# Kernel tuning notes

Measured on AMD Instinct MI355X. Metric: run time of the kernel, lower is better.

Reference implementation:

```python
import jax, jax.numpy as jnp
import numpy as np

B, T, I, H, L, C = 8192, 50, 50, 10, 3, 5


def setup_inputs() -> dict:
    key = jax.random.key(0)
    ks = jax.random.split(key, 20)
    s = 1.0 / np.sqrt(H)  # torch nn.RNN init scale
    inp = {
        "x": jax.random.normal(ks[0], (B, T, I), dtype=jnp.float32),
        "h0": jax.random.normal(ks[1], (L, B, H), dtype=jnp.float32),
    }
    # per-layer weights: layer 0 takes input_size I, layers 1,2 take H
    in_sizes = [I, H, H]
    for l in range(L):
        inp[f"W_ih{l}"] = jax.random.uniform(ks[2 + 4 * l], (H, in_sizes[l]), minval=-s, maxval=s, dtype=jnp.float32)
        inp[f"W_hh{l}"] = jax.random.uniform(ks[3 + 4 * l], (H, H), minval=-s, maxval=s, dtype=jnp.float32)
        inp[f"b_ih{l}"] = jax.random.uniform(ks[4 + 4 * l], (H,), minval=-s, maxval=s, dtype=jnp.float32)
        inp[f"b_hh{l}"] = jax.random.uniform(ks[5 + 4 * l], (H,), minval=-s, maxval=s, dtype=jnp.float32)
    sf = 1.0 / np.sqrt(H * T)
    inp["fc_w"] = jax.random.uniform(ks[14], (C, H * T), minval=-sf, maxval=sf, dtype=jnp.float32)
    inp["fc_b"] = jax.random.uniform(ks[15], (C,), minval=-sf, maxval=sf, dtype=jnp.float32)
    return inp


def _rnn_layer(x, h0, W_ih, b_ih, W_hh, b_hh):
    # x: [B, T, in], h0: [B, H]. h_t = tanh(x_t W_ih^T + b_ih + h_{t-1} W_hh^T + b_hh)
    xW = jnp.einsum("bti,hi->bth", x, W_ih) + (b_ih + b_hh)  # input proj precomputed

    def step(h, xw_t):
        h = jnp.tanh(xw_t + h @ W_hh.T)
        return h, h

    _, ys = jax.lax.scan(step, h0, jnp.swapaxes(xW, 0, 1))  # ys: [T, B, H]
    return jnp.swapaxes(ys, 0, 1)  # [B, T, H]


def reference(x, h0, W_ih0, W_hh0, b_ih0, b_hh0, W_ih1, W_hh1, b_ih1, b_hh1,
              W_ih2, W_hh2, b_ih2, b_hh2, fc_w, fc_b):
    layers = [(W_ih0, b_ih0, W_hh0, b_hh0),
              (W_ih1, b_ih1, W_hh1, b_hh1),
              (W_ih2, b_ih2, W_hh2, b_hh2)]
    out = x
    for l, (Wi, bi, Wh, bh) in enumerate(layers):
        out = _rnn_layer(out, h0[l], Wi, bi, Wh, bh)
    flat = jax.nn.relu(out.reshape(out.shape[0], -1))  # [B, T*H]
    return flat @ fc_w.T + fc_b  # [B, C]
```

## Files before the change

kernel.cpp:

```cpp
#include <hip/hip_runtime.h>

#define BB 8192
#define TT 50
#define II 50
#define HH 10
#define CC 5

__device__ __forceinline__ float fast_tanh(float x) {
    float e = __expf(2.0f * x);
    return 1.0f - 2.0f * __builtin_amdgcn_rcpf(e + 1.0f);
}

__global__ __launch_bounds__(256) void k_proj0(
    const float* __restrict__ x, const float* __restrict__ Wih0,
    const float* __restrict__ bih0, const float* __restrict__ bhh0,
    float* __restrict__ P) {
    int gid = blockIdx.x * 256 + threadIdx.x;
    int b = gid & (BB - 1);
    int t = gid >> 13;
    const float2* xr = (const float2*)(x + ((size_t)b * TT + t) * II);
    float2 xv[II / 2];
#pragma unroll
    for (int i = 0; i < II / 2; i++) xv[i] = xr[i];
#pragma unroll
    for (int j = 0; j < HH; j++) {
        float a = bih0[j] + bhh0[j];
        const float2* w = (const float2*)(Wih0 + j * II);
#pragma unroll
        for (int i = 0; i < II / 2; i++) {
            float2 wv = w[i];
            a = fmaf(wv.x, xv[i].x, a);
            a = fmaf(wv.y, xv[i].y, a);
        }
        P[((size_t)t * HH + j) * BB + b] = a;
    }
}

__global__ __launch_bounds__(256, 4) void k_fused(
    const float* __restrict__ h0all,
    const float* __restrict__ Whh0,
    const float* __restrict__ Wih1, const float* __restrict__ Whh1,
    const float* __restrict__ bih1, const float* __restrict__ bhh1,
    const float* __restrict__ Wih2, const float* __restrict__ Whh2,
    const float* __restrict__ bih2, const float* __restrict__ bhh2,
    const float* __restrict__ fcw, const float* __restrict__ fcb,
    const float* __restrict__ P, float* __restrict__ out) {
    __shared__ float sfcT[TT * HH * CC];
    __shared__ __align__(16) float sh[2][3][16][12];

    const int tid = threadIdx.x;
    const int j = tid & 15;
    const int g16 = tid >> 4;
    const int b = blockIdx.x * 16 + g16;
    const bool jv = (j < HH);

    for (int idx = tid; idx < TT * HH * CC; idx += 256) {
        int r = idx / CC, c = idx - r * CC;
        sfcT[idx] = fcw[(size_t)c * (TT * HH) + r];
    }

    float w0[HH], wi1[HH], wh1[HH], wi2[HH], wh2[HH];
    float bs1 = 0.0f, bs2 = 0.0f, h1i = 0.0f, h2i = 0.0f;
    if (jv) {
#pragma unroll
        for (int k = 0; k < HH; k++) {
            w0[k]  = Whh0[j * HH + k];
            wi1[k] = Wih1[j * HH + k];
            wh1[k] = Whh1[j * HH + k];
            wi2[k] = Wih2[j * HH + k];
            wh2[k] = Whh2[j * HH + k];
        }
        bs1 = bih1[j] + bhh1[j];
        bs2 = bih2[j] + bhh2[j];
        h1i = h0all[(size_t)BB * HH + (size_t)b * HH + j];
        h2i = h0all[(size_t)2 * BB * HH + (size_t)b * HH + j];
    } else {
#pragma unroll
        for (int k = 0; k < HH; k++) {
            w0[k] = wi1[k] = wh1[k] = wi2[k] = wh2[k] = 0.0f;
        }
    }

    if (j < 12) {
        float h0i = jv ? h0all[(size_t)b * HH + j] : 0.0f;
        sh[1][0][g16][j] = h0i;
        sh[1][1][g16][j] = (j < HH) ? h1i : 0.0f;
        sh[1][2][g16][j] = (j < HH) ? h2i : 0.0f;
    }

    __syncthreads();

    float acc[CC] = {0.0f, 0.0f, 0.0f, 0.0f, 0.0f};
    float pc = jv ? P[(size_t)j * BB + b] : 0.0f;
    float p1 = jv ? P[(size_t)(((1 < TT) ? 1 : TT - 1) * HH + j) * BB + b] : 0.0f;

#pragma unroll 1
    for (int i = 0; i < TT + 2; i++) {
        const int pr = (i + 1) & 1;
        const int pw = i & 1;

        int tp = (i + 2 < TT) ? (i + 2) : (TT - 1);
        float p2 = jv ? P[(size_t)(tp * HH + j) * BB + b] : 0.0f;

        float hv0[HH], hv1[HH], hv2[HH];
        {
            const float* b0 = &sh[pr][0][g16][0];
            const float* b1 = &sh[pr][1][g16][0];
            const float* b2 = &sh[pr][2][g16][0];
            float4 a4 = *(const float4*)(b0);
            float4 b4 = *(const float4*)(b0 + 4);
            float2 c2 = *(const float2*)(b0 + 8);
            hv0[0] = a4.x; hv0[1] = a4.y; hv0[2] = a4.z; hv0[3] = a4.w;
            hv0[4] = b4.x; hv0[5] = b4.y; hv0[6] = b4.z; hv0[7] = b4.w;
            hv0[8] = c2.x; hv0[9] = c2.y;
            a4 = *(const float4*)(b1); b4 = *(const float4*)(b1 + 4); c2 = *(const float2*)(b1 + 8);
            hv1[0] = a4.x; hv1[1] = a4.y; hv1[2] = a4.z; hv1[3] = a4.w;
            hv1[4] = b4.x; hv1[5] = b4.y; hv1[6] = b4.z; hv1[7] = b4.w;
            hv1[8] = c2.x; hv1[9] = c2.y;
            a4 = *(const float4*)(b2); b4 = *(const float4*)(b2 + 4); c2 = *(const float2*)(b2 + 8);
            hv2[0] = a4.x; hv2[1] = a4.y; hv2[2] = a4.z; hv2[3] = a4.w;
            hv2[4] = b4.x; hv2[5] = b4.y; hv2[6] = b4.z; hv2[7] = b4.w;
            hv2[8] = c2.x; hv2[9] = c2.y;
        }

        float a0 = pc, a1 = bs1, a2 = bs2;
#pragma unroll
        for (int k = 0; k < HH; k++) {
            a0 = fmaf(w0[k],  hv0[k], a0);
            a1 = fmaf(wi1[k], hv0[k], a1);
            a1 = fmaf(wh1[k], hv1[k], a1);
            a2 = fmaf(wi2[k], hv1[k], a2);
            a2 = fmaf(wh2[k], hv2[k], a2);
        }
        float h0o = fast_tanh(a0);
        float h1o = fast_tanh(a1);
        float h2o = fast_tanh(a2);

        if (i >= 2 && jv) {
            float rl = fmaxf(h2o, 0.0f);
            int base = ((i - 2) * HH + j) * CC;
#pragma unroll
            for (int c = 0; c < CC; c++) acc[c] = fmaf(sfcT[base + c], rl, acc[c]);
        }

        if (j < 12) {
            float v1 = (i == 0) ? h1i : h1o;
            float v2 = (i <= 1) ? h2i : h2o;
            sh[pw][0][g16][j] = h0o;
            sh[pw][1][g16][j] = v1;
            sh[pw][2][g16][j] = v2;
        }
        pc = p1;
        p1 = p2;
    }

#pragma unroll
    for (int c = 0; c < CC; c++) {
        float a = acc[c];
        a += __shfl_xor(a, 1);
        a += __shfl_xor(a, 2);
        a += __shfl_xor(a, 4);
        a += __shfl_xor(a, 8);
        acc[c] = a + fcb[c];
    }
    if (j == 0) {
#pragma unroll
        for (int c = 0; c < CC; c++) out[(size_t)b * CC + c] = acc[c];
    }
}

extern "C" void kernel_launch(void* const* d_in, const int* in_sizes, int n_in,
                              void* d_out, int out_size, void* d_ws, size_t ws_size,
                              hipStream_t stream) {
    const float* x    = (const float*)d_in[0];
    const float* h0   = (const float*)d_in[1];
    const float* Wih0 = (const float*)d_in[2];
    const float* Whh0 = (const float*)d_in[3];
    const float* bih0 = (const float*)d_in[4];
    const float* bhh0 = (const float*)d_in[5];
    const float* Wih1 = (const float*)d_in[6];
    const float* Whh1 = (const float*)d_in[7];
    const float* bih1 = (const float*)d_in[8];
    const float* bhh1 = (const float*)d_in[9];
    const float* Wih2 = (const float*)d_in[10];
    const float* Whh2 = (const float*)d_in[11];
    const float* bih2 = (const float*)d_in[12];
    const float* bhh2 = (const float*)d_in[13];
    const float* fcw  = (const float*)d_in[14];
    const float* fcb  = (const float*)d_in[15];
    float* out = (float*)d_out;
    float* P   = (float*)d_ws;

    k_proj0<<<(BB * TT) / 256, 256, 0, stream>>>(x, Wih0, bih0, bhh0, P);
    k_fused<<<BB / 16, 256, 0, stream>>>(h0, Whh0, Wih1, Whh1, bih1, bhh1,
                                         Wih2, Whh2, bih2, bhh2, fcw, fcb, P, out);
}
```

Before: 55.54 us.

## Broadcast hidden state via ds_swizzle instead of LDS double buffer

Replaces the shared-memory double-buffered hidden-state exchange with ds_swizzle broadcasts within each 16-lane group, so every lane reads all 10 hidden values straight from registers. This removes the LDS stores and vector loads on the recurrence's critical path. The P prefetch is deepened from 2 to 4 steps, and the fc weights are padded to stride 8 so each step can use one float4 load. Launch bounds drop the occupancy hint from 4 to 2 blocks, which allows more registers at the cost of fewer resident waves.

Result: slower. 64.15 us (+15.5%).

```diff
diff --git a/kernel.cpp b/kernel.cpp
--- a/kernel.cpp
+++ b/kernel.cpp
@@ -10,6 +10,14 @@
     float e = __expf(2.0f * x);
     return 1.0f - 2.0f * __builtin_amdgcn_rcpf(e + 1.0f);
 }
+
+#define SWZ(x, K) __uint_as_float((unsigned)__builtin_amdgcn_ds_swizzle( \
+    (int)__float_as_uint(x), (((K) << 5) | 0x10)))
+#define BC10(H, src)                                                     \
+    H[0] = SWZ(src, 0); H[1] = SWZ(src, 1); H[2] = SWZ(src, 2);          \
+    H[3] = SWZ(src, 3); H[4] = SWZ(src, 4); H[5] = SWZ(src, 5);          \
+    H[6] = SWZ(src, 6); H[7] = SWZ(src, 7); H[8] = SWZ(src, 8);          \
+    H[9] = SWZ(src, 9);
 
 __global__ __launch_bounds__(256) void k_proj0(
     const float* __restrict__ x, const float* __restrict__ Wih0,
@@ -36,7 +44,7 @@
     }
 }
 
-__global__ __launch_bounds__(256, 4) void k_fused(
+__global__ __launch_bounds__(256, 2) void k_fused(
     const float* __restrict__ h0all,
     const float* __restrict__ Whh0,
     const float* __restrict__ Wih1, const float* __restrict__ Whh1,
@@ -45,8 +53,7 @@
     const float* __restrict__ bih2, const float* __restrict__ bhh2,
     const float* __restrict__ fcw, const float* __restrict__ fcb,
     const float* __restrict__ P, float* __restrict__ out) {
-    __shared__ float sfcT[TT * HH * CC];
-    __shared__ __align__(16) float sh[2][3][16][12];
+    __shared__ __align__(16) float sfc8[TT * HH * 8];
 
     const int tid = threadIdx.x;
     const int j = tid & 15;
@@ -54,13 +61,13 @@
     const int b = blockIdx.x * 16 + g16;
     const bool jv = (j < HH);
 
-    for (int idx = tid; idx < TT * HH * CC; idx += 256) {
-        int r = idx / CC, c = idx - r * CC;
-        sfcT[idx] = fcw[(size_t)c * (TT * HH) + r];
+    for (int idx = tid; idx < TT * HH * 8; idx += 256) {
+        int r = idx >> 3, c = idx & 7;
+        sfc8[idx] = (c < CC) ? fcw[(size_t)c * (TT * HH) + r] : 0.0f;
     }
 
     float w0[HH], wi1[HH], wh1[HH], wi2[HH], wh2[HH];
-    float bs1 = 0.0f, bs2 = 0.0f, h1i = 0.0f, h2i = 0.0f;
+    float bs1 = 0.0f, bs2 = 0.0f, h1i = 0.0f, h2i = 0.0f, h0i = 0.0f;
     if (jv) {
 #pragma unroll
         for (int k = 0; k < HH; k++) {
@@ -72,6 +79,7 @@
         }
         bs1 = bih1[j] + bhh1[j];
         bs2 = bih2[j] + bhh2[j];
+        h0i = h0all[(size_t)b * HH + j];
         h1i = h0all[(size_t)BB * HH + (size_t)b * HH + j];
         h2i = h0all[(size_t)2 * BB * HH + (size_t)b * HH + j];
     } else {
@@ -81,77 +89,58 @@
         }
     }
 
-    if (j < 12) {
-        float h0i = jv ? h0all[(size_t)b * HH + j] : 0.0f;
-        sh[1][0][g16][j] = h0i;
-        sh[1][1][g16][j] = (j < HH) ? h1i : 0.0f;
-        sh[1][2][g16][j] = (j < HH) ? h2i : 0.0f;
-    }
-
     __syncthreads();
 
+    float h0o = h0i, h1o = h1i, h2o = h2i;
+
     float acc[CC] = {0.0f, 0.0f, 0.0f, 0.0f, 0.0f};
-    float pc = jv ? P[(size_t)j * BB + b] : 0.0f;
-    float p1 = jv ? P[(size_t)(((1 < TT) ? 1 : TT - 1) * HH + j) * BB + b] : 0.0f;
+
+    float p0 = jv ? P[(size_t)(0 * HH + j) * BB + b] : 0.0f;
+    float p1 = jv ? P[(size_t)(1 * HH + j) * BB + b] : 0.0f;
+    float p2 = jv ? P[(size_t)(2 * HH + j) * BB + b] : 0.0f;
+    float p3 = jv ? P[(size_t)(3 * HH + j) * BB + b] : 0.0f;
 
 #pragma unroll 1
     for (int i = 0; i < TT + 2; i++) {
-        const int pr = (i + 1) & 1;
-        const int pw = i & 1;
+        float H0[HH], H1[HH], H2[HH];
+        BC10(H0, h0o)
+        BC10(H1, h1o)
+        BC10(H2, h2o)
 
-        int tp = (i + 2 < TT) ? (i + 2) : (TT - 1);
-        float p2 = jv ? P[(size_t)(tp * HH + j) * BB + b] : 0.0f;
+        int tp = (i + 4 < TT) ? (i + 4) : (TT - 1);
+        float pnew = jv ? P[(size_t)(tp * HH + j) * BB + b] : 0.0f;
 
-        float hv0[HH], hv1[HH], hv2[HH];
-        {
-            const float* b0 = &sh[pr][0][g16][0];
-            const float* b1 = &sh[pr][1][g16][0];
-            const float* b2 = &sh[pr][2][g16][0];
-            float4 a4 = *(const float4*)(b0);
-            float4 b4 = *(const float4*)(b0 + 4);
-            float2 c2 = *(const float2*)(b0 + 8);
-            hv0[0] = a4.x; hv0[1] = a4.y; hv0[2] = a4.z; hv0[3] = a4.w;
-            hv0[4] = b4.x; hv0[5] = b4.y; hv0[6] = b4.z; hv0[7] = b4.w;
-            hv0[8] = c2.x; hv0[9] = c2.y;
-            a4 = *(const float4*)(b1); b4 = *(const float4*)(b1 + 4); c2 = *(const float2*)(b1 + 8);
-            hv1[0] = a4.x; hv1[1] = a4.y; hv1[2] = a4.z; hv1[3] = a4.w;
-            hv1[4] = b4.x; hv1[5] = b4.y; hv1[6] = b4.z; hv1[7] = b4.w;
-            hv1[8] = c2.x; hv1[9] = c2.y;
-            a4 = *(const float4*)(b2); b4 = *(const float4*)(b2 + 4); c2 = *(const float2*)(b2 + 8);
-            hv2[0] = a4.x; hv2[1] = a4.y; hv2[2] = a4.z; hv2[3] = a4.w;
-            hv2[4] = b4.x; hv2[5] = b4.y; hv2[6] = b4.z; hv2[7] = b4.w;
-            hv2[8] = c2.x; hv2[9] = c2.y;
+        int tauc = (i >= 2) ? (i - 2) : 0;
+        const float* fb = &sfc8[(tauc * HH + j) * 8];
+        float4 f4 = *(const float4*)fb;
+        float  f1 = fb[4];
+
+        float a0 = p0, a1 = bs1, a2 = bs2;
+#pragma unroll
+        for (int k = 0; k < HH; k++) {
+            a0 = fmaf(w0[k],  H0[k], a0);
+            a1 = fmaf(wi1[k], H0[k], a1);
+            a1 = fmaf(wh1[k], H1[k], a1);
+            a2 = fmaf(wi2[k], H1[k], a2);
+            a2 = fmaf(wh2[k], H2[k], a2);
+        }
+        float t0 = fast_tanh(a0);
+        float t1 = fast_tanh(a1);
+        float t2 = fast_tanh(a2);
+
+        if (i >= 2 && jv) {
+            float rl = fmaxf(t2, 0.0f);
+            acc[0] = fmaf(f4.x, rl, acc[0]);
+            acc[1] = fmaf(f4.y, rl, acc[1]);
+            acc[2] = fmaf(f4.z, rl, acc[2]);
+            acc[3] = fmaf(f4.w, rl, acc[3]);
+            acc[4] = fmaf(f1,  rl, acc[4]);
         }
 
-        float a0 = pc, a1 = bs1, a2 = bs2;
-#pragma unroll
-        for (int k = 0; k < HH; k++) {
-            a0 = fmaf(w0[k],  hv0[k], a0);
-            a1 = fmaf(wi1[k], hv0[k], a1);
-            a1 = fmaf(wh1[k], hv1[k], a1);
-            a2 = fmaf(wi2[k], hv1[k], a2);
-            a2 = fmaf(wh2[k], hv2[k], a2);
-        }
-        float h0o = fast_tanh(a0);
-        float h1o = fast_tanh(a1);
-        float h2o = fast_tanh(a2);
-
-        if (i >= 2 && jv) {
-            float rl = fmaxf(h2o, 0.0f);
-            int base = ((i - 2) * HH + j) * CC;
-#pragma unroll
-            for (int c = 0; c < CC; c++) acc[c] = fmaf(sfcT[base + c], rl, acc[c]);
-        }
-
-        if (j < 12) {
-            float v1 = (i == 0) ? h1i : h1o;
-            float v2 = (i <= 1) ? h2i : h2o;
-            sh[pw][0][g16][j] = h0o;
-            sh[pw][1][g16][j] = v1;
-            sh[pw][2][g16][j] = v2;
-        }
-        pc = p1;
-        p1 = p2;
+        h0o = t0;
+        h1o = (i == 0) ? h1i : t1;
+        h2o = (i <= 1) ? h2i : t2;
+        p0 = p1; p1 = p2; p2 = p3; p3 = pnew;
     }
 
 #pragma unroll
```
